# Performance work log

Hardware: AMD Instinct MI355X
Metric: run time of the kernel (lower is better)

The kernel has to match this reference:

```python
import jax, jax.numpy as jnp
import numpy as np

B, S, H, D = 2, 4096, 16, 128
TILE = 128
T = S // TILE          # 32 tiles
TOPK = 7               # anchor-selected tiles per query tile (local tile appended -> 8)
DM = H * D
NEG = -1e10


def setup_inputs() -> dict:
    key = jax.random.key(0)
    ks = jax.random.split(key, 6)
    x = jax.random.normal(ks[0], (B, S, DM), dtype=jnp.float32)
    wq = jax.random.normal(ks[1], (DM, H * D), dtype=jnp.float32) * 0.02
    wk = jax.random.normal(ks[2], (DM, H * D), dtype=jnp.float32) * 0.02
    wv = jax.random.normal(ks[3], (DM, H * D), dtype=jnp.float32) * 0.02
    wo = jax.random.normal(ks[4], (H * D, DM), dtype=jnp.float32) * 0.02
    # RoPE tables (real/imag of freqs_cis), LLaMA-style
    inv_freq = 1.0 / (10000.0 ** (np.arange(0, D, 2, dtype=np.float32) / D))  # [D/2]
    t = np.arange(S, dtype=np.float32)
    freqs = np.outer(t, inv_freq)  # [S, D/2]
    cos = jnp.asarray(np.cos(freqs), dtype=jnp.float32)
    sin = jnp.asarray(np.sin(freqs), dtype=jnp.float32)
    anchor_indices = jax.random.randint(ks[5], (B, H, T, TOPK), 0, T, dtype=jnp.int32)
    return {"x": x, "wq": wq, "wk": wk, "wv": wv, "wo": wo,
            "cos": cos, "sin": sin, "anchor_indices": anchor_indices}


def _apply_rope(q, k, cos, sin):
    # q,k: [B,H,S,D]; cos,sin: [S,D/2]
    cos_f = jnp.concatenate([cos, cos], axis=-1)[None, None]  # [1,1,S,D]
    sin_f = jnp.concatenate([sin, sin], axis=-1)[None, None]

    def rot_half(x):
        h = x.shape[-1] // 2
        return jnp.concatenate([-x[..., h:], x[..., :h]], axis=-1)

    return q * cos_f + rot_half(q) * sin_f, k * cos_f + rot_half(k) * sin_f


def reference(x, wq, wk, wv, wo, cos, sin, anchor_indices):
    b, s, _ = x.shape
    h = anchor_indices.shape[1]
    t = anchor_indices.shape[2]
    tile = s // t
    d = wq.shape[1] // h

    q = (x @ wq).reshape(b, s, h, d).transpose(0, 2, 1, 3)  # [B,H,S,D]
    k = (x @ wk).reshape(b, s, h, d).transpose(0, 2, 1, 3)
    v = (x @ wv).reshape(b, s, h, d).transpose(0, 2, 1, 3)
    q, k = _apply_rope(q, k, cos, sin)

    # append local tile to anchor-selected tiles -> [B,H,T,K+1]
    local = jnp.broadcast_to(jnp.arange(t, dtype=jnp.int32)[None, None, :, None], (b, h, t, 1))
    tile_sel = jnp.concatenate([anchor_indices, local], axis=-1)
    # token indices of gathered tiles: [B,H,T,(K+1)*tile]
    offs = jnp.arange(tile, dtype=jnp.int32)[None, None, None, None, :]
    tok_idx = (tile_sel[..., None] * tile + offs)
    sparse_len = tile_sel.shape[-1] * tile
    flat_idx = jnp.clip(tok_idx.reshape(b, h, t, sparse_len), 0, s - 1)

    # gather K/V tiles: [B,H,T,L,D]
    gid = flat_idx.reshape(b, h, t * sparse_len)
    k_sp = jnp.take_along_axis(k, gid[..., None], axis=2).reshape(b, h, t, sparse_len, d)
    v_sp = jnp.take_along_axis(v, gid[..., None], axis=2).reshape(b, h, t, sparse_len, d)

    q_t = q.reshape(b, h, t, tile, d)
    logits = jnp.einsum('bhtqd,bhtkd->bhtqk', q_t, k_sp) / jnp.sqrt(jnp.float32(d))

    # causal future-mask within gathered set
    q_pos = jnp.arange(s, dtype=jnp.int32).reshape(t, tile)
    fut = flat_idx[:, :, :, None, :] > q_pos[None, None, :, :, None]  # [B,H,T,tile,L]
    logits = jnp.where(fut, NEG, logits)
    weights = jax.nn.softmax(logits, axis=-1)
    all_masked = jnp.all(fut, axis=-1, keepdims=True)
    weights = jnp.where(all_masked, 0.0, weights)
    weights = jnp.where(jnp.isnan(weights), 0.0, weights)

    out = jnp.einsum('bhtqk,bhtkd->bhtqd', weights, v_sp)
    out = out.reshape(b, h, s, d).transpose(0, 2, 1, 3).reshape(b, s, h * d)
    return out @ wo
```

## Files before the change

### kernel.cpp

```cpp
#include <hip/hip_runtime.h>
#include <hip/hip_bf16.h>


typedef __bf16 bf16_t;
using bf16x8 = __attribute__((ext_vector_type(8))) __bf16;
using bf16x4 = __attribute__((ext_vector_type(4))) __bf16;
using f32x4  = __attribute__((ext_vector_type(4))) float;

typedef const __attribute__((address_space(1))) void* gas_ptr;
typedef __attribute__((address_space(3))) void* las_ptr;

__device__ __forceinline__ void async_copy16(const void* g, void* l) {
  __builtin_amdgcn_global_load_lds((gas_ptr)g, (las_ptr)l, 16, 0, 0);
}

__device__ __forceinline__ f32x4 mfma16x16x32(bf16x8 a, bf16x8 b, f32x4 c) {
  return __builtin_amdgcn_mfma_f32_16x16x32_bf16(a, b, c, 0, 0, 0);
}

__global__ void cvt_f32_bf16(const float* __restrict__ X, bf16_t* __restrict__ Y) {
  int idx = blockIdx.x * 256 + threadIdx.x;
  float4 v = ((const float4*)X)[idx];
  bf16x4 r;
  r.x = (bf16_t)v.x; r.y = (bf16_t)v.y; r.z = (bf16_t)v.z; r.w = (bf16_t)v.w;
  ((bf16x4*)Y)[idx] = r;
}

__global__ void wtrans(const float* __restrict__ W, bf16_t* __restrict__ Wt) {
  __shared__ bf16_t t[64][66];
  const int r0 = blockIdx.x * 64, c0 = blockIdx.y * 64;
  const int tx = threadIdx.x & 63, ty = threadIdx.x >> 6;
  #pragma unroll
  for (int i = 0; i < 16; ++i) {
    int r = ty + 4 * i;
    t[r][tx] = (bf16_t)W[(size_t)(r0 + r) * 2048 + c0 + tx];
  }
  __syncthreads();
  #pragma unroll
  for (int i = 0; i < 16; ++i) {
    int n = ty + 4 * i;
    Wt[(size_t)(c0 + n) * 2048 + r0 + tx] = t[tx][n];
  }
}

__global__ __launch_bounds__(512, 2) void gemm256(
    const bf16_t* __restrict__ A, const bf16_t* __restrict__ Bt,
    int nb, int mode, float* __restrict__ Cf,
    bf16_t* __restrict__ outQ, bf16_t* __restrict__ outK,
    bf16_t* __restrict__ outVT,
    const float* __restrict__ cosT, const float* __restrict__ sinT)
{
  __shared__ bf16_t Apan[2][16384];
  __shared__ bf16_t Bpan[2][16384];
  const int bid = blockIdx.x;
  const int cpx = gridDim.x >> 3;
  const int swz = (bid & 7) * cpx + (bid >> 3);
  const int bm = (swz / nb) * 256, bn = (swz % nb) * 256;
  const int tid = threadIdx.x;
  const int w = tid >> 6, l = tid & 63;
  const int wr = w >> 1, wc = w & 1;
  const int fr = l & 15, g4 = l >> 4;

  const bf16_t* aS[4];
  const bf16_t* bS[4];
  int dst[4];
  #pragma unroll
  for (int i = 0; i < 4; ++i) {
    int c = tid + i * 512;
    int row = c >> 3, ch = c & 7;
    int sc = (ch ^ (row & 7)) * 8;
    aS[i] = A  + (size_t)(bm + row) * 2048 + sc;
    bS[i] = Bt + (size_t)(bn + row) * 2048 + sc;
    dst[i] = c * 16;
  }

  int aOff[2][4], bOff[2][8];
  #pragma unroll
  for (int kc = 0; kc < 2; ++kc) {
    #pragma unroll
    for (int m = 0; m < 4; ++m) {
      int R = wr * 64 + m * 16 + fr;
      aOff[kc][m] = R * 128 + (((kc * 4 + g4) ^ (R & 7)) << 4);
    }
    #pragma unroll
    for (int n = 0; n < 8; ++n) {
      int R = wc * 128 + n * 16 + fr;
      bOff[kc][n] = R * 128 + (((kc * 4 + g4) ^ (R & 7)) << 4);
    }
  }

  f32x4 acc[4][8];
  #pragma unroll
  for (int m = 0; m < 4; ++m)
    #pragma unroll
    for (int n = 0; n < 8; ++n) acc[m][n] = (f32x4){0.f, 0.f, 0.f, 0.f};

  auto STAGE = [&](int t) {
    const int slot = t & 1;
    const int kb = t * 64;
    char* dA = (char*)&Apan[slot][0];
    char* dB = (char*)&Bpan[slot][0];
    #pragma unroll
    for (int i = 0; i < 4; ++i) {
      async_copy16(aS[i] + kb, dA + dst[i]);
      async_copy16(bS[i] + kb, dB + dst[i]);
    }
  };

  STAGE(0);
  __syncthreads();

  #pragma unroll 1
  for (int phi = 0; phi < 32; ++phi) {
    const int slot = phi & 1;
    const char* pa = (const char*)&Apan[slot][0];
    const char* pb = (const char*)&Bpan[slot][0];

    bf16x8 af0[4], bf0[8];
    #pragma unroll
    for (int m = 0; m < 4; ++m) af0[m] = *(const bf16x8*)(pa + aOff[0][m]);
    #pragma unroll
    for (int n = 0; n < 8; ++n) bf0[n] = *(const bf16x8*)(pb + bOff[0][n]);
    if (phi < 31) STAGE(phi + 1);
    __builtin_amdgcn_s_setprio(1);
    #pragma unroll
    for (int m = 0; m < 4; ++m)
      #pragma unroll
      for (int n = 0; n < 8; ++n)
        acc[m][n] = mfma16x16x32(af0[m], bf0[n], acc[m][n]);
    __builtin_amdgcn_s_setprio(0);

    bf16x8 af1[4], bf1[8];
    #pragma unroll
    for (int m = 0; m < 4; ++m) af1[m] = *(const bf16x8*)(pa + aOff[1][m]);
    #pragma unroll
    for (int n = 0; n < 8; ++n) bf1[n] = *(const bf16x8*)(pb + bOff[1][n]);
    __builtin_amdgcn_s_setprio(1);
    #pragma unroll
    for (int m = 0; m < 4; ++m)
      #pragma unroll
      for (int n = 0; n < 8; ++n)
        acc[m][n] = mfma16x16x32(af1[m], bf1[n], acc[m][n]);
    __builtin_amdgcn_s_setprio(0);

    asm volatile("s_waitcnt vmcnt(0)" ::: "memory");
    __builtin_amdgcn_sched_barrier(0);
    __builtin_amdgcn_s_barrier();
    __builtin_amdgcn_sched_barrier(0);
  }

  if (mode == 0) {
    #pragma unroll
    for (int m = 0; m < 4; ++m)
      #pragma unroll
      for (int n = 0; n < 8; ++n)
        #pragma unroll
        for (int j = 0; j < 4; ++j) {
          int row = bm + wr * 64 + m * 16 + g4 * 4 + j;
          int col = bn + wc * 128 + n * 16 + fr;
          Cf[(size_t)row * 2048 + col] = acc[m][n][j];
        }
    return;
  }

  const int colbase = bn + wc * 128;
  const int proj = colbase >> 11;
  const int hh = (colbase & 2047) >> 7;
  if (proj == 2) {
    #pragma unroll
    for (int m = 0; m < 4; ++m) {
      int row0 = bm + wr * 64 + m * 16 + g4 * 4;
      int b_ = row0 >> 12, sr = row0 & 4095;
      #pragma unroll
      for (int n = 0; n < 8; ++n) {
        int d_ = n * 16 + fr;
        bf16x4 pkv;
        #pragma unroll
        for (int j = 0; j < 4; ++j) pkv[j] = (bf16_t)acc[m][n][j];
        *(bf16x4*)&outVT[(((size_t)(b_ * 16 + hh)) * 128 + d_) * 4096 + sr] = pkv;
      }
    }
  } else {
    bf16_t* dst_ = proj ? outK : outQ;
    #pragma unroll
    for (int m = 0; m < 4; ++m) {
      int row0 = bm + wr * 64 + m * 16 + g4 * 4;
      int b_ = row0 >> 12, s0 = row0 & 4095;
      size_t hbase = ((size_t)(b_ * 16 + hh)) * 4096;
      #pragma unroll
      for (int n = 0; n < 4; ++n) {
        int d = n * 16 + fr;
        #pragma unroll
        for (int j = 0; j < 4; ++j) {
          int s = s0 + j;
          float c  = cosT[s * 64 + d];
          float sn = sinT[s * 64 + d];
          float x0 = acc[m][n][j], x1 = acc[m][n + 4][j];
          dst_[(hbase + s) * 128 + d]      = (bf16_t)(x0 * c - x1 * sn);
          dst_[(hbase + s) * 128 + d + 64] = (bf16_t)(x1 * c + x0 * sn);
        }
      }
    }
  }
}

__global__ __launch_bounds__(512, 4) void attn_kernel(
    const bf16_t* __restrict__ Qf, const bf16_t* __restrict__ Kf,
    const bf16_t* __restrict__ Vt, const int* __restrict__ anchors,
    bf16_t* __restrict__ outB)
{
  __shared__ bf16_t Kl[2][8192];
  __shared__ bf16_t Vl[2][8192];
  __shared__ bf16_t Pbuf[8][1024];
  const int orig = blockIdx.x;
  const int blk = (orig & 7) * 128 + (orig >> 3);
  const int qt = 31 - (blk & 31);
  const int h = (blk >> 5) & 15, b = blk >> 9;
  const int bh = b * 16 + h;
  const int tid = threadIdx.x, w = tid >> 6, l = tid & 63;
  const int fr = l & 15, g4 = l >> 4;
  const float scale = 0.08838834764831845f;

  const int* anc = anchors + ((size_t)bh * 32 + qt) * 7;
  unsigned long long pk = 0;
  int nt = 0;
  #pragma unroll
  for (int t = 0; t < 7; ++t) {
    int v = anc[t];
    if (v <= qt) { pk |= (unsigned long long)v << (5 * nt); ++nt; }
  }
  pk |= (unsigned long long)qt << (5 * nt); ++nt;
  const int NS = nt * 2;

  const bf16_t* Qbase = Qf + (size_t)bh * 4096 * 128;
  const bf16_t* Kbase = Kf + (size_t)bh * 4096 * 128;
  const bf16_t* Vbase = Vt + (size_t)bh * 128 * 4096;
  char* P = (char*)&Pbuf[w][0];

  auto STAGE = [&](int tb2, int p) {
    const bf16_t* ksrc = Kbase + (size_t)tb2 * 128;
    const bf16_t* vsrc = Vbase + tb2;
    char* kd = (char*)&Kl[p][0];
    char* vd = (char*)&Vl[p][0];
    #pragma unroll
    for (int i = 0; i < 2; ++i) {
      int c = tid + i * 512;
      int kr = c >> 4, kcol = c & 15;
      async_copy16(ksrc + (size_t)kr * 128 + (size_t)((kcol ^ (kr & 7)) * 8),
                   kd + c * 16);
      int vr = c >> 3, vcol = c & 7;
      async_copy16(vsrc + (size_t)vr * 4096 + (size_t)((vcol ^ (vr & 7)) * 8),
                   vd + c * 16);
    }
  };

  const int qrow = qt * 128 + w * 16 + fr;
  bf16x8 aq[4];
  #pragma unroll
  for (int kc = 0; kc < 4; ++kc)
    aq[kc] = *(const bf16x8*)(Qbase + (size_t)qrow * 128 + kc * 32 + g4 * 8);

  STAGE((int)(pk & 31) * 128, 0);
  __syncthreads();

  float mrun = -1e30f, lrun = 0.f;
  f32x4 o[8];
  #pragma unroll
  for (int nd = 0; nd < 8; ++nd) o[nd] = (f32x4){0.f, 0.f, 0.f, 0.f};

  for (int s = 0; s < NS; ++s) {
    const int p = s & 1;
    const int ts = (int)((pk >> (5 * (s >> 1))) & 31);
    const bool domask = (ts == qt);
    if (s + 1 < NS) {
      int s1 = s + 1;
      int ts1 = (int)((pk >> (5 * (s1 >> 1))) & 31);
      STAGE(ts1 * 128 + (s1 & 1) * 64, p ^ 1);
    }

    f32x4 sc[4];
    #pragma unroll
    for (int n = 0; n < 4; ++n) sc[n] = (f32x4){0.f, 0.f, 0.f, 0.f};
    #pragma unroll
    for (int kc = 0; kc < 4; ++kc) {
      bf16x8 kf[4];
      #pragma unroll
      for (int n = 0; n < 4; ++n) {
        int r = n * 16 + fr;
        kf[n] = *(const bf16x8*)((const char*)&Kl[p][0] +
                 r * 256 + (((kc * 4 + g4) ^ (r & 7)) << 4));
      }
      #pragma unroll
      for (int n = 0; n < 4; ++n)
        sc[n] = mfma16x16x32(kf[n], aq[kc], sc[n]);
    }

    float rmax = -1e30f;
    if (domask) {
      const int qr = w * 16 + fr;
      #pragma unroll
      for (int n = 0; n < 4; ++n)
        #pragma unroll
        for (int j = 0; j < 4; ++j) {
          float lg = sc[n][j] * scale;
          int tok = (s & 1) * 64 + n * 16 + g4 * 4 + j;
          if (tok > qr) lg = -1e10f;
          sc[n][j] = lg;
          rmax = fmaxf(rmax, lg);
        }
    } else {
      #pragma unroll
      for (int n = 0; n < 4; ++n)
        #pragma unroll
        for (int j = 0; j < 4; ++j) {
          float lg = sc[n][j] * scale;
          sc[n][j] = lg;
          rmax = fmaxf(rmax, lg);
        }
    }
    rmax = fmaxf(rmax, __shfl_xor(rmax, 16));
    rmax = fmaxf(rmax, __shfl_xor(rmax, 32));
    if (__any(rmax > mrun + 8.f)) {
      float mnew = fmaxf(mrun, rmax);
      float alpha = __expf(mrun - mnew);
      lrun *= alpha;
      #pragma unroll
      for (int nd = 0; nd < 8; ++nd)
        #pragma unroll
        for (int j = 0; j < 4; ++j) o[nd][j] *= alpha;
      mrun = mnew;
    }
    float rsum = 0.f;
    #pragma unroll
    for (int n = 0; n < 4; ++n) {
      bf16x4 pkv;
      #pragma unroll
      for (int j = 0; j < 4; ++j) {
        float pe = __expf(sc[n][j] - mrun);
        rsum += pe;
        pkv[j] = (bf16_t)pe;
      }
      int off = fr * 128 + ((((n << 1) | (g4 >> 1)) ^ (fr & 7)) << 4) + ((g4 & 1) << 3);
      *(bf16x4*)(P + off) = pkv;
    }
    rsum += __shfl_xor(rsum, 16);
    rsum += __shfl_xor(rsum, 32);
    lrun += rsum;

    #pragma unroll
    for (int kc2 = 0; kc2 < 2; ++kc2) {
      bf16x8 av[8];
      #pragma unroll
      for (int nd = 0; nd < 8; ++nd) {
        int r = nd * 16 + fr;
        av[nd] = *(const bf16x8*)((const char*)&Vl[p][0] +
                  r * 128 + (((kc2 * 4 + g4) ^ (r & 7)) << 4));
      }
      bf16x8 bp = *(const bf16x8*)(P + fr * 128 + ((((kc2 << 2) | g4) ^ (fr & 7)) << 4));
      #pragma unroll
      for (int nd = 0; nd < 8; ++nd)
        o[nd] = mfma16x16x32(av[nd], bp, o[nd]);
    }
    __syncthreads();
  }

  {
    char* E = (char*)&Kl[0][0] + w * 4096;
    float inv = 1.0f / lrun;
    #pragma unroll
    for (int nd = 0; nd < 8; ++nd) {
      bf16x4 pkv;
      #pragma unroll
      for (int j = 0; j < 4; ++j) pkv[j] = (bf16_t)(o[nd][j] * inv);
      int off = fr * 256 + ((((nd << 1) | (g4 >> 1)) ^ (fr & 7)) << 4) + ((g4 & 1) << 3);
      *(bf16x4*)(E + off) = pkv;
    }
    #pragma unroll
    for (int i = 0; i < 4; ++i) {
      int r = i * 4 + g4;
      int off = r * 256 + ((fr ^ (r & 7)) << 4);
      bf16x8 vrow = *(const bf16x8*)(E + off);
      size_t gaddr = (((size_t)b * 4096 + qt * 128 + w * 16 + r) * 2048)
                     + h * 128 + fr * 8;
      *(bf16x8*)(outB + gaddr) = vrow;
    }
  }
}

#define OFF_XB   ((size_t)0)
#define OFF_WCAT ((size_t)33554432)
#define OFF_WOT  ((size_t)58720256)
#define OFF_QF   ((size_t)67108864)
#define OFF_KF   ((size_t)100663296)
#define OFF_AT   ((size_t)134217728)
#define OFF_VT   ((size_t)167772160)

extern "C" void kernel_launch(void* const* d_in, const int* in_sizes, int n_in,
                              void* d_out, int out_size, void* d_ws, size_t ws_size,
                              hipStream_t stream) {
  (void)in_sizes; (void)n_in; (void)out_size; (void)ws_size;
  const float* x    = (const float*)d_in[0];
  const float* wq   = (const float*)d_in[1];
  const float* wk   = (const float*)d_in[2];
  const float* wv   = (const float*)d_in[3];
  const float* wo   = (const float*)d_in[4];
  const float* cosT = (const float*)d_in[5];
  const float* sinT = (const float*)d_in[6];
  const int*   anc  = (const int*)d_in[7];
  float* out = (float*)d_out;
  char* ws = (char*)d_ws;

  bf16_t* xb   = (bf16_t*)(ws + OFF_XB);
  bf16_t* wcat = (bf16_t*)(ws + OFF_WCAT);
  bf16_t* wqt  = wcat;
  bf16_t* wkt  = wcat + (size_t)2048 * 2048;
  bf16_t* wvt  = wcat + (size_t)4096 * 2048;
  bf16_t* wot  = (bf16_t*)(ws + OFF_WOT);
  bf16_t* Qf   = (bf16_t*)(ws + OFF_QF);
  bf16_t* Kf   = (bf16_t*)(ws + OFF_KF);
  bf16_t* Vt   = (bf16_t*)(ws + OFF_VT);
  bf16_t* attnB = (bf16_t*)(ws + OFF_AT);

  cvt_f32_bf16<<<16384, 256, 0, stream>>>(x, xb);
  wtrans<<<dim3(32, 32), 256, 0, stream>>>(wq, wqt);
  wtrans<<<dim3(32, 32), 256, 0, stream>>>(wk, wkt);
  wtrans<<<dim3(32, 32), 256, 0, stream>>>(wv, wvt);
  wtrans<<<dim3(32, 32), 256, 0, stream>>>(wo, wot);
  gemm256<<<768, 512, 0, stream>>>(xb, wcat, 24, 1, nullptr, Qf, Kf, Vt, cosT, sinT);
  attn_kernel<<<1024, 512, 0, stream>>>(Qf, Kf, Vt, anc, attnB);
  gemm256<<<256, 512, 0, stream>>>(attnB, wot, 8, 0, out, nullptr, nullptr, nullptr,
                                   nullptr, nullptr);
}
```

Baseline: 369.3 us.

## Shrink attention KV stage to 32 tokens and merge weight transposes

The attention kernel now streams K/V in 32-token chunks instead of 64, which halves the LDS footprint (a single 40KB buffer) so more workgroups can be resident per CU. The cost is twice as many pipeline steps and barriers, and fewer MFMAs per step. The four weight-transpose launches are also merged into one 3D-grid launch to cut launch overhead.

Result: no change. 375.6 us (+1.7%).

```diff
diff --git a/kernel.cpp b/kernel.cpp
--- a/kernel.cpp
+++ b/kernel.cpp
@@ -26,8 +26,13 @@
   ((bf16x4*)Y)[idx] = r;
 }
 
-__global__ void wtrans(const float* __restrict__ W, bf16_t* __restrict__ Wt) {
+__global__ void wtrans4(const float* __restrict__ wq, const float* __restrict__ wk,
+                        const float* __restrict__ wv, const float* __restrict__ wo,
+                        bf16_t* __restrict__ wcat, bf16_t* __restrict__ wot) {
   __shared__ bf16_t t[64][66];
+  const int z = blockIdx.z;
+  const float* W = (z == 0) ? wq : (z == 1) ? wk : (z == 2) ? wv : wo;
+  bf16_t* Wt = (z == 3) ? wot : (wcat + (size_t)z * 2048 * 2048);
   const int r0 = blockIdx.x * 64, c0 = blockIdx.y * 64;
   const int tx = threadIdx.x & 63, ty = threadIdx.x >> 6;
   #pragma unroll
@@ -209,9 +214,10 @@
     const bf16_t* __restrict__ Vt, const int* __restrict__ anchors,
     bf16_t* __restrict__ outB)
 {
-  __shared__ bf16_t Kl[2][8192];
-  __shared__ bf16_t Vl[2][8192];
-  __shared__ bf16_t Pbuf[8][1024];
+  __shared__ bf16_t SH[20480];
+  bf16_t* Klb = SH;
+  bf16_t* Vlb = SH + 8192;
+  bf16_t* Pb  = SH + 16384;
   const int orig = blockIdx.x;
   const int blk = (orig & 7) * 128 + (orig >> 3);
   const int qt = 31 - (blk & 31);
@@ -230,28 +236,24 @@
     if (v <= qt) { pk |= (unsigned long long)v << (5 * nt); ++nt; }
   }
   pk |= (unsigned long long)qt << (5 * nt); ++nt;
-  const int NS = nt * 2;
+  const int NS = nt * 4;
 
   const bf16_t* Qbase = Qf + (size_t)bh * 4096 * 128;
   const bf16_t* Kbase = Kf + (size_t)bh * 4096 * 128;
   const bf16_t* Vbase = Vt + (size_t)bh * 128 * 4096;
-  char* P = (char*)&Pbuf[w][0];
+  char* P = (char*)(Pb + w * 512);
 
   auto STAGE = [&](int tb2, int p) {
     const bf16_t* ksrc = Kbase + (size_t)tb2 * 128;
     const bf16_t* vsrc = Vbase + tb2;
-    char* kd = (char*)&Kl[p][0];
-    char* vd = (char*)&Vl[p][0];
-    #pragma unroll
-    for (int i = 0; i < 2; ++i) {
-      int c = tid + i * 512;
-      int kr = c >> 4, kcol = c & 15;
-      async_copy16(ksrc + (size_t)kr * 128 + (size_t)((kcol ^ (kr & 7)) * 8),
-                   kd + c * 16);
-      int vr = c >> 3, vcol = c & 7;
-      async_copy16(vsrc + (size_t)vr * 4096 + (size_t)((vcol ^ (vr & 7)) * 8),
-                   vd + c * 16);
-    }
+    char* kd = (char*)(Klb + p * 4096);
+    char* vd = (char*)(Vlb + p * 4096);
+    int kr = tid >> 4, kcol = tid & 15;
+    async_copy16(ksrc + (size_t)kr * 128 + (size_t)((kcol ^ (kr & 7)) * 8),
+                 kd + tid * 16);
+    int vr = tid >> 2, vcol = tid & 3;
+    async_copy16(vsrc + (size_t)vr * 4096 + (size_t)((vcol ^ (vr & 3)) * 8),
+                 vd + tid * 16);
   };
 
   const int qrow = qt * 128 + w * 16 + fr;
@@ -270,47 +272,47 @@
 
   for (int s = 0; s < NS; ++s) {
     const int p = s & 1;
-    const int ts = (int)((pk >> (5 * (s >> 1))) & 31);
+    const int ts = (int)((pk >> (5 * (s >> 2))) & 31);
+    const int qq = s & 3;
     const bool domask = (ts == qt);
     if (s + 1 < NS) {
       int s1 = s + 1;
-      int ts1 = (int)((pk >> (5 * (s1 >> 1))) & 31);
-      STAGE(ts1 * 128 + (s1 & 1) * 64, p ^ 1);
-    }
-
-    f32x4 sc[4];
-    #pragma unroll
-    for (int n = 0; n < 4; ++n) sc[n] = (f32x4){0.f, 0.f, 0.f, 0.f};
+      int ts1 = (int)((pk >> (5 * (s1 >> 2))) & 31);
+      STAGE(ts1 * 128 + (s1 & 3) * 32, p ^ 1);
+    }
+
+    const char* Klp = (const char*)(Klb + p * 4096);
+    f32x4 sc[2];
+    sc[0] = (f32x4){0.f, 0.f, 0.f, 0.f};
+    sc[1] = (f32x4){0.f, 0.f, 0.f, 0.f};
     #pragma unroll
     for (int kc = 0; kc < 4; ++kc) {
-      bf16x8 kf[4];
-      #pragma unroll
-      for (int n = 0; n < 4; ++n) {
+      bf16x8 kf[2];
+      #pragma unroll
+      for (int n = 0; n < 2; ++n) {
         int r = n * 16 + fr;
-        kf[n] = *(const bf16x8*)((const char*)&Kl[p][0] +
-                 r * 256 + (((kc * 4 + g4) ^ (r & 7)) << 4));
+        kf[n] = *(const bf16x8*)(Klp + r * 256 + (((kc * 4 + g4) ^ (r & 7)) << 4));
       }
-      #pragma unroll
-      for (int n = 0; n < 4; ++n)
-        sc[n] = mfma16x16x32(kf[n], aq[kc], sc[n]);
+      sc[0] = mfma16x16x32(kf[0], aq[kc], sc[0]);
+      sc[1] = mfma16x16x32(kf[1], aq[kc], sc[1]);
     }
 
     float rmax = -1e30f;
     if (domask) {
       const int qr = w * 16 + fr;
       #pragma unroll
-      for (int n = 0; n < 4; ++n)
+      for (int n = 0; n < 2; ++n)
         #pragma unroll
         for (int j = 0; j < 4; ++j) {
           float lg = sc[n][j] * scale;
-          int tok = (s & 1) * 64 + n * 16 + g4 * 4 + j;
+          int tok = qq * 32 + n * 16 + g4 * 4 + j;
           if (tok > qr) lg = -1e10f;
           sc[n][j] = lg;
           rmax = fmaxf(rmax, lg);
         }
     } else {
       #pragma unroll
-      for (int n = 0; n < 4; ++n)
+      for (int n = 0; n < 2; ++n)
         #pragma unroll
         for (int j = 0; j < 4; ++j) {
           float lg = sc[n][j] * scale;
@@ -332,7 +334,7 @@
     }
     float rsum = 0.f;
     #pragma unroll
-    for (int n = 0; n < 4; ++n) {
+    for (int n = 0; n < 2; ++n) {
       bf16x4 pkv;
       #pragma unroll
       for (int j = 0; j < 4; ++j) {
@@ -340,23 +342,22 @@
         rsum += pe;
         pkv[j] = (bf16_t)pe;
       }
-      int off = fr * 128 + ((((n << 1) | (g4 >> 1)) ^ (fr & 7)) << 4) + ((g4 & 1) << 3);
+      int off = fr * 64 + ((((n << 1) | (g4 >> 1)) ^ (fr & 3)) << 4) + ((g4 & 1) << 3);
       *(bf16x4*)(P + off) = pkv;
     }
     rsum += __shfl_xor(rsum, 16);
     rsum += __shfl_xor(rsum, 32);
     lrun += rsum;
 
-    #pragma unroll
-    for (int kc2 = 0; kc2 < 2; ++kc2) {
+    {
+      const char* Vlp = (const char*)(Vlb + p * 4096);
       bf16x8 av[8];
       #pragma unroll
       for (int nd = 0; nd < 8; ++nd) {
         int r = nd * 16 + fr;
-        av[nd] = *(const bf16x8*)((const char*)&Vl[p][0] +
-                  r * 128 + (((kc2 * 4 + g4) ^ (r & 7)) << 4));
+        av[nd] = *(const bf16x8*)(Vlp + r * 64 + ((g4 ^ (r & 3)) << 4));
       }
-      bf16x8 bp = *(const bf16x8*)(P + fr * 128 + ((((kc2 << 2) | g4) ^ (fr & 7)) << 4));
+      bf16x8 bp = *(const bf16x8*)(P + fr * 64 + ((g4 ^ (fr & 3)) << 4));
       #pragma unroll
       for (int nd = 0; nd < 8; ++nd)
         o[nd] = mfma16x16x32(av[nd], bp, o[nd]);
@@ -365,7 +366,7 @@
   }
 
   {
-    char* E = (char*)&Kl[0][0] + w * 4096;
+    char* E = (char*)SH + w * 4096;
     float inv = 1.0f / lrun;
     #pragma unroll
     for (int nd = 0; nd < 8; ++nd) {
@@ -412,9 +413,6 @@
 
   bf16_t* xb   = (bf16_t*)(ws + OFF_XB);
   bf16_t* wcat = (bf16_t*)(ws + OFF_WCAT);
-  bf16_t* wqt  = wcat;
-  bf16_t* wkt  = wcat + (size_t)2048 * 2048;
-  bf16_t* wvt  = wcat + (size_t)4096 * 2048;
   bf16_t* wot  = (bf16_t*)(ws + OFF_WOT);
   bf16_t* Qf   = (bf16_t*)(ws + OFF_QF);
   bf16_t* Kf   = (bf16_t*)(ws + OFF_KF);
@@ -422,10 +420,7 @@
   bf16_t* attnB = (bf16_t*)(ws + OFF_AT);
 
   cvt_f32_bf16<<<16384, 256, 0, stream>>>(x, xb);
-  wtrans<<<dim3(32, 32), 256, 0, stream>>>(wq, wqt);
-  wtrans<<<dim3(32, 32), 256, 0, stream>>>(wk, wkt);
-  wtrans<<<dim3(32, 32), 256, 0, stream>>>(wv, wvt);
-  wtrans<<<dim3(32, 32), 256, 0, stream>>>(wo, wot);
+  wtrans4<<<dim3(32, 32, 4), 256, 0, stream>>>(wq, wk, wv, wo, wcat, wot);
   gemm256<<<768, 512, 0, stream>>>(xb, wcat, 24, 1, nullptr, Qf, Kf, Vt, cosT, sinT);
   attn_kernel<<<1024, 512, 0, stream>>>(Qf, Kf, Vt, anc, attnB);
   gemm256<<<256, 512, 0, stream>>>(attnB, wot, 8, 0, out, nullptr, nullptr, nullptr,
```
